# Optimization experiments

Measured on AMD Instinct MI355X. Metric: run time of the kernel, lower is better.

Reference implementation:

```python
import jax, jax.numpy as jnp
import numpy as np

SIZE = 7  # spatial size, matches init kwarg


def setup_inputs() -> dict:
    key = jax.random.key(0)
    k1, k2 = jax.random.split(key, 2)
    N, C, H, W = 256, 2048, SIZE, SIZE
    x = jax.random.normal(k1, (N, C, H, W), dtype=jnp.float32)
    # nn.Linear(2*C, 2): weight (2, 2C), bias (2,)
    Wlin = jax.random.normal(k2, (2, 2 * C), dtype=jnp.float32) * 0.02
    b = jnp.zeros((2,), dtype=jnp.float32)
    return {"x": x, "Wlin": Wlin, "b": b}


def reference(x, Wlin, b):
    N, C, H, W = x.shape
    HW = H * W
    size = SIZE
    # (N, HW, C) token view
    rx = x.reshape(N, C, HW).transpose(0, 2, 1)
    # index of max mean-activation token per sample
    idx = jnp.argmax(jnp.mean(rx, axis=-1), axis=-1)  # (N,)
    bidx = jnp.arange(N)
    max_feat = rx[bidx, idx]  # (N, C)
    # concat(max_feat, rx) @ Wlin.T + b, split to avoid materializing (N,HW,2C)
    W1, W2 = Wlin[:, :C], Wlin[:, C:]
    pred = jax.nn.relu(
        jnp.einsum('npc,oc->npo', rx, W2) + (max_feat @ W1.T)[:, None, :] + b
    )  # (N, HW, 2)
    # zero out prediction at the anchor token
    pred = pred.at[bidx, idx].set(0.0)
    # basic label grid (i, j)
    ii, jj = jnp.meshgrid(jnp.arange(H), jnp.arange(W), indexing='ij')
    label = jnp.stack([ii, jj], axis=-1).reshape(HW, 2).astype(x.dtype)  # (HW, 2)
    anchor = label[idx][:, None, :]  # (N, 1, 2)
    rel = (label[None, :, :] - anchor) / size  # (N, HW, 2)
    rel_dist = jnp.sqrt(jnp.sum(rel ** 2, axis=-1))  # (N, HW)
    rel_angle = (jnp.arctan2(rel[..., 1], rel[..., 0]) / jnp.pi + 1) / 2  # (N, HW)
    dist_loss = (pred[..., 0] - rel_dist) ** 2
    gap = pred[..., 1] - rel_angle
    gap = jnp.where(gap < 0, gap + 1, gap)
    gap = gap - jnp.mean(gap, axis=-1, keepdims=True)
    return (dist_loss + gap ** 2).reshape(N, H, W)
```

## Files before the change

### kernel.cpp

```cpp
#include <hip/hip_runtime.h>
#include <hip/hip_bf16.h>
#include <math.h>

#define N_BATCH 256
#define C_CH    2048
#define HW      49
#define SIZE7   7
#define S_SPLIT 8
#define C_PER   (C_CH / S_SPLIT)
#define BLOCK   256
#define WAVES   4

__global__ __launch_bounds__(BLOCK) void rpp_partial_kernel(
    const float* __restrict__ x, const float* __restrict__ Wlin,
    float* __restrict__ ws) {
  const int bid  = blockIdx.x;
  const int n    = bid >> 3;
  const int s    = bid & (S_SPLIT - 1);
  const int tid  = threadIdx.x;
  const int lane = tid & 63;
  const int wave = tid >> 6;

  __shared__ __align__(16) float w_s[4][C_PER];
  __shared__ float red[WAVES][5][64];

  const int cbase = s * C_PER;
  for (int i = tid; i < 4 * C_PER; i += BLOCK) {
    const int q = i >> 8;
    const int c = i & (C_PER - 1);
    const int off = (q & 1) * (2 * C_CH) + (q >> 1) * C_CH;
    w_s[q][c] = Wlin[off + cbase + c];
  }
  __syncthreads();

  const int lp = (lane < HW) ? lane : 0;
  const int wbase = wave * 64;
  const float* xp = x + (size_t)n * C_CH * HW + (size_t)(cbase + wbase) * HW + lp;

  float a0 = 0.f, a1 = 0.f, a2 = 0.f, a3 = 0.f, a4 = 0.f;
#pragma unroll 4
  for (int c = 0; c < 64; c += 4, xp += 4 * HW) {
    const float v0 = xp[0 * HW];
    const float v1 = xp[1 * HW];
    const float v2 = xp[2 * HW];
    const float v3 = xp[3 * HW];
    const float4 w0 = *(const float4*)&w_s[0][wbase + c];
    const float4 w1 = *(const float4*)&w_s[1][wbase + c];
    const float4 w2 = *(const float4*)&w_s[2][wbase + c];
    const float4 w3 = *(const float4*)&w_s[3][wbase + c];
    a0 += (v0 + v1) + (v2 + v3);
    a1 = fmaf(v0, w0.x, fmaf(v1, w0.y, fmaf(v2, w0.z, fmaf(v3, w0.w, a1))));
    a2 = fmaf(v0, w1.x, fmaf(v1, w1.y, fmaf(v2, w1.z, fmaf(v3, w1.w, a2))));
    a3 = fmaf(v0, w2.x, fmaf(v1, w2.y, fmaf(v2, w2.z, fmaf(v3, w2.w, a3))));
    a4 = fmaf(v0, w3.x, fmaf(v1, w3.y, fmaf(v2, w3.z, fmaf(v3, w3.w, a4))));
  }

  red[wave][0][lane] = a0;
  red[wave][1][lane] = a1;
  red[wave][2][lane] = a2;
  red[wave][3][lane] = a3;
  red[wave][4][lane] = a4;
  __syncthreads();

  for (int i = tid; i < 5 * 64; i += BLOCK) {
    const int q = i >> 6;
    const int l = i & 63;
    ws[(size_t)bid * 320 + i] =
        red[0][q][l] + red[1][q][l] + red[2][q][l] + red[3][q][l];
  }
}

__global__ __launch_bounds__(64) void rpp_final_kernel(
    const float* __restrict__ ws, const float* __restrict__ b,
    float* __restrict__ out) {
  const int n = blockIdx.x;
  const int lane = threadIdx.x;

  float s0 = 0.f, s1 = 0.f, s2 = 0.f, s3 = 0.f, s4 = 0.f;
  const float* base = ws + (size_t)n * S_SPLIT * 320;
#pragma unroll
  for (int s = 0; s < S_SPLIT; s++) {
    const float* bs = base + s * 320;
    s0 += bs[0 * 64 + lane];
    s1 += bs[1 * 64 + lane];
    s2 += bs[2 * 64 + lane];
    s3 += bs[3 * 64 + lane];
    s4 += bs[4 * 64 + lane];
  }

  float v = (lane < HW) ? s0 : -INFINITY;
  int vi = lane;
#pragma unroll
  for (int off = 32; off; off >>= 1) {
    const float ov = __shfl_down(v, off);
    const int oi = __shfl_down(vi, off);
    if (ov > v || (ov == v && oi < vi)) { v = ov; vi = oi; }
  }
  const int idx = __shfl(vi, 0);

  const float anc0 = __shfl(s1, idx);
  const float anc1 = __shfl(s2, idx);
  const float b0 = b[0], b1 = b[1];

  float pred0 = fmaxf(s3 + anc0 + b0, 0.f);
  float pred1 = fmaxf(s4 + anc1 + b1, 0.f);
  if (lane == idx) { pred0 = 0.f; pred1 = 0.f; }

  const int li = lane / SIZE7, lj = lane % SIZE7;
  const int ai = idx / SIZE7, aj = idx % SIZE7;
  const float ri = (float)(li - ai) * (1.0f / SIZE7);
  const float rj = (float)(lj - aj) * (1.0f / SIZE7);
  const float rdist = sqrtf(ri * ri + rj * rj);
  const float rangle = atan2f(rj, ri) * 0.15915494309189535f + 0.5f;

  float dl = pred0 - rdist;
  dl *= dl;
  float gap = pred1 - rangle;
  if (gap < 0.f) gap += 1.f;

  float g = (lane < HW) ? gap : 0.f;
#pragma unroll
  for (int off = 32; off; off >>= 1) g += __shfl_down(g, off);
  const float mean = __shfl(g, 0) * (1.0f / HW);
  gap -= mean;

  if (lane < HW) out[(size_t)n * HW + lane] = dl + gap * gap;
}

extern "C" void kernel_launch(void* const* d_in, const int* in_sizes, int n_in,
                              void* d_out, int out_size, void* d_ws, size_t ws_size,
                              hipStream_t stream) {
  const float* x    = (const float*)d_in[0];
  const float* Wlin = (const float*)d_in[1];
  const float* b    = (const float*)d_in[2];
  float* out = (float*)d_out;
  float* ws  = (float*)d_ws;

  hipLaunchKernelGGL(rpp_partial_kernel, dim3(N_BATCH * S_SPLIT), dim3(BLOCK), 0,
                     stream, x, Wlin, ws);
  hipLaunchKernelGGL(rpp_final_kernel, dim3(N_BATCH), dim3(64), 0,
                     stream, ws, b, out);
}
```

Measured before the change: 154.9 us.

## Fuse partial reduction and final loss into one 1024-thread block per sample

Replaces the split-channel partial kernel plus the final kernel with a single kernel in which one 1024-thread block handles a whole sample. The cross-block reduction moves into shared memory and the workspace round trip goes away. The inner loop is unrolled to eight channels per iteration. This removes a launch and the global intermediate, but leaves only one block per CU with fewer resident waves to hide memory latency.

```diff
diff --git a/kernel.cpp b/kernel.cpp
--- a/kernel.cpp
+++ b/kernel.cpp
@@ -1,58 +1,66 @@
 #include <hip/hip_runtime.h>
-#include <hip/hip_bf16.h>
 #include <math.h>
 
 #define N_BATCH 256
 #define C_CH    2048
 #define HW      49
 #define SIZE7   7
-#define S_SPLIT 8
-#define C_PER   (C_CH / S_SPLIT)
-#define BLOCK   256
-#define WAVES   4
+#define BLOCK   1024
+#define NWAVES  16
+#define C_PER_W (C_CH / NWAVES)
 
-__global__ __launch_bounds__(BLOCK) void rpp_partial_kernel(
+__global__ __launch_bounds__(BLOCK) void rpp_fused_kernel(
     const float* __restrict__ x, const float* __restrict__ Wlin,
-    float* __restrict__ ws) {
-  const int bid  = blockIdx.x;
-  const int n    = bid >> 3;
-  const int s    = bid & (S_SPLIT - 1);
+    const float* __restrict__ b, float* __restrict__ out) {
+  const int n    = blockIdx.x;
   const int tid  = threadIdx.x;
   const int lane = tid & 63;
   const int wave = tid >> 6;
 
-  __shared__ __align__(16) float w_s[4][C_PER];
-  __shared__ float red[WAVES][5][64];
+  __shared__ __align__(16) float w_s[4][C_CH];
+  __shared__ float red[NWAVES][5][64];
 
-  const int cbase = s * C_PER;
-  for (int i = tid; i < 4 * C_PER; i += BLOCK) {
-    const int q = i >> 8;
-    const int c = i & (C_PER - 1);
+  for (int i = tid; i < 4 * C_CH; i += BLOCK) {
+    const int q = i >> 11;
+    const int c = i & (C_CH - 1);
     const int off = (q & 1) * (2 * C_CH) + (q >> 1) * C_CH;
-    w_s[q][c] = Wlin[off + cbase + c];
+    w_s[q][c] = Wlin[off + c];
   }
   __syncthreads();
 
   const int lp = (lane < HW) ? lane : 0;
-  const int wbase = wave * 64;
-  const float* xp = x + (size_t)n * C_CH * HW + (size_t)(cbase + wbase) * HW + lp;
+  const int cb = wave * C_PER_W;
+  const float* xp = x + (size_t)n * C_CH * HW + (size_t)cb * HW + lp;
 
   float a0 = 0.f, a1 = 0.f, a2 = 0.f, a3 = 0.f, a4 = 0.f;
-#pragma unroll 4
-  for (int c = 0; c < 64; c += 4, xp += 4 * HW) {
+#pragma unroll 2
+  for (int c = 0; c < C_PER_W; c += 8) {
     const float v0 = xp[0 * HW];
     const float v1 = xp[1 * HW];
     const float v2 = xp[2 * HW];
     const float v3 = xp[3 * HW];
-    const float4 w0 = *(const float4*)&w_s[0][wbase + c];
-    const float4 w1 = *(const float4*)&w_s[1][wbase + c];
-    const float4 w2 = *(const float4*)&w_s[2][wbase + c];
-    const float4 w3 = *(const float4*)&w_s[3][wbase + c];
-    a0 += (v0 + v1) + (v2 + v3);
-    a1 = fmaf(v0, w0.x, fmaf(v1, w0.y, fmaf(v2, w0.z, fmaf(v3, w0.w, a1))));
-    a2 = fmaf(v0, w1.x, fmaf(v1, w1.y, fmaf(v2, w1.z, fmaf(v3, w1.w, a2))));
-    a3 = fmaf(v0, w2.x, fmaf(v1, w2.y, fmaf(v2, w2.z, fmaf(v3, w2.w, a3))));
-    a4 = fmaf(v0, w3.x, fmaf(v1, w3.y, fmaf(v2, w3.z, fmaf(v3, w3.w, a4))));
+    const float v4 = xp[4 * HW];
+    const float v5 = xp[5 * HW];
+    const float v6 = xp[6 * HW];
+    const float v7 = xp[7 * HW];
+    xp += 8 * HW;
+    const float4 wa0 = *(const float4*)&w_s[0][cb + c];
+    const float4 wa1 = *(const float4*)&w_s[0][cb + c + 4];
+    const float4 wb0 = *(const float4*)&w_s[1][cb + c];
+    const float4 wb1 = *(const float4*)&w_s[1][cb + c + 4];
+    const float4 wc0 = *(const float4*)&w_s[2][cb + c];
+    const float4 wc1 = *(const float4*)&w_s[2][cb + c + 4];
+    const float4 wd0 = *(const float4*)&w_s[3][cb + c];
+    const float4 wd1 = *(const float4*)&w_s[3][cb + c + 4];
+    a0 += ((v0 + v1) + (v2 + v3)) + ((v4 + v5) + (v6 + v7));
+    a1 = fmaf(v0, wa0.x, fmaf(v1, wa0.y, fmaf(v2, wa0.z, fmaf(v3, wa0.w, a1))));
+    a1 = fmaf(v4, wa1.x, fmaf(v5, wa1.y, fmaf(v6, wa1.z, fmaf(v7, wa1.w, a1))));
+    a2 = fmaf(v0, wb0.x, fmaf(v1, wb0.y, fmaf(v2, wb0.z, fmaf(v3, wb0.w, a2))));
+    a2 = fmaf(v4, wb1.x, fmaf(v5, wb1.y, fmaf(v6, wb1.z, fmaf(v7, wb1.w, a2))));
+    a3 = fmaf(v0, wc0.x, fmaf(v1, wc0.y, fmaf(v2, wc0.z, fmaf(v3, wc0.w, a3))));
+    a3 = fmaf(v4, wc1.x, fmaf(v5, wc1.y, fmaf(v6, wc1.z, fmaf(v7, wc1.w, a3))));
+    a4 = fmaf(v0, wd0.x, fmaf(v1, wd0.y, fmaf(v2, wd0.z, fmaf(v3, wd0.w, a4))));
+    a4 = fmaf(v4, wd1.x, fmaf(v5, wd1.y, fmaf(v6, wd1.z, fmaf(v7, wd1.w, a4))));
   }
 
   red[wave][0][lane] = a0;
@@ -62,69 +70,61 @@
   red[wave][4][lane] = a4;
   __syncthreads();
 
-  for (int i = tid; i < 5 * 64; i += BLOCK) {
-    const int q = i >> 6;
-    const int l = i & 63;
-    ws[(size_t)bid * 320 + i] =
-        red[0][q][l] + red[1][q][l] + red[2][q][l] + red[3][q][l];
+  if (tid < 5 * 64) {
+    const int q = tid >> 6;
+    const int l = tid & 63;
+    float s = 0.f;
+#pragma unroll
+    for (int w = 0; w < NWAVES; w++) s += red[w][q][l];
+    red[0][q][l] = s;
   }
-}
+  __syncthreads();
 
-__global__ __launch_bounds__(64) void rpp_final_kernel(
-    const float* __restrict__ ws, const float* __restrict__ b,
-    float* __restrict__ out) {
-  const int n = blockIdx.x;
-  const int lane = threadIdx.x;
+  if (wave == 0) {
+    const float s0 = red[0][0][lane];
+    const float s1 = red[0][1][lane];
+    const float s2 = red[0][2][lane];
+    const float s3 = red[0][3][lane];
+    const float s4 = red[0][4][lane];
 
-  float s0 = 0.f, s1 = 0.f, s2 = 0.f, s3 = 0.f, s4 = 0.f;
-  const float* base = ws + (size_t)n * S_SPLIT * 320;
+    float v = (lane < HW) ? s0 : -INFINITY;
+    int vi = lane;
 #pragma unroll
-  for (int s = 0; s < S_SPLIT; s++) {
-    const float* bs = base + s * 320;
-    s0 += bs[0 * 64 + lane];
-    s1 += bs[1 * 64 + lane];
-    s2 += bs[2 * 64 + lane];
-    s3 += bs[3 * 64 + lane];
-    s4 += bs[4 * 64 + lane];
+    for (int off = 32; off; off >>= 1) {
+      const float ov = __shfl_down(v, off);
+      const int oi = __shfl_down(vi, off);
+      if (ov > v || (ov == v && oi < vi)) { v = ov; vi = oi; }
+    }
+    const int idx = __shfl(vi, 0);
+
+    const float anc0 = __shfl(s1, idx);
+    const float anc1 = __shfl(s2, idx);
+    const float b0 = b[0], b1 = b[1];
+
+    float pred0 = fmaxf(s3 + anc0 + b0, 0.f);
+    float pred1 = fmaxf(s4 + anc1 + b1, 0.f);
+    if (lane == idx) { pred0 = 0.f; pred1 = 0.f; }
+
+    const int li = lane / SIZE7, lj = lane % SIZE7;
+    const int ai = idx / SIZE7, aj = idx % SIZE7;
+    const float ri = (float)(li - ai) * (1.0f / SIZE7);
+    const float rj = (float)(lj - aj) * (1.0f / SIZE7);
+    const float rdist = sqrtf(ri * ri + rj * rj);
+    const float rangle = atan2f(rj, ri) * 0.15915494309189535f + 0.5f;
+
+    float dl = pred0 - rdist;
+    dl *= dl;
+    float gap = pred1 - rangle;
+    if (gap < 0.f) gap += 1.f;
+
+    float g = (lane < HW) ? gap : 0.f;
+#pragma unroll
+    for (int off = 32; off; off >>= 1) g += __shfl_down(g, off);
+    const float mean = __shfl(g, 0) * (1.0f / HW);
+    gap -= mean;
+
+    if (lane < HW) out[(size_t)n * HW + lane] = dl + gap * gap;
   }
-
-  float v = (lane < HW) ? s0 : -INFINITY;
-  int vi = lane;
-#pragma unroll
-  for (int off = 32; off; off >>= 1) {
-    const float ov = __shfl_down(v, off);
-    const int oi = __shfl_down(vi, off);
-    if (ov > v || (ov == v && oi < vi)) { v = ov; vi = oi; }
-  }
-  const int idx = __shfl(vi, 0);
-
-  const float anc0 = __shfl(s1, idx);
-  const float anc1 = __shfl(s2, idx);
-  const float b0 = b[0], b1 = b[1];
-
-  float pred0 = fmaxf(s3 + anc0 + b0, 0.f);
-  float pred1 = fmaxf(s4 + anc1 + b1, 0.f);
-  if (lane == idx) { pred0 = 0.f; pred1 = 0.f; }
-
-  const int li = lane / SIZE7, lj = lane % SIZE7;
-  const int ai = idx / SIZE7, aj = idx % SIZE7;
-  const float ri = (float)(li - ai) * (1.0f / SIZE7);
-  const float rj = (float)(lj - aj) * (1.0f / SIZE7);
-  const float rdist = sqrtf(ri * ri + rj * rj);
-  const float rangle = atan2f(rj, ri) * 0.15915494309189535f + 0.5f;
-
-  float dl = pred0 - rdist;
-  dl *= dl;
-  float gap = pred1 - rangle;
-  if (gap < 0.f) gap += 1.f;
-
-  float g = (lane < HW) ? gap : 0.f;
-#pragma unroll
-  for (int off = 32; off; off >>= 1) g += __shfl_down(g, off);
-  const float mean = __shfl(g, 0) * (1.0f / HW);
-  gap -= mean;
-
-  if (lane < HW) out[(size_t)n * HW + lane] = dl + gap * gap;
 }
 
 extern "C" void kernel_launch(void* const* d_in, const int* in_sizes, int n_in,
@@ -134,10 +134,8 @@
   const float* Wlin = (const float*)d_in[1];
   const float* b    = (const float*)d_in[2];
   float* out = (float*)d_out;
-  float* ws  = (float*)d_ws;
+  (void)d_ws; (void)ws_size;
 
-  hipLaunchKernelGGL(rpp_partial_kernel, dim3(N_BATCH * S_SPLIT), dim3(BLOCK), 0,
-                     stream, x, Wlin, ws);
-  hipLaunchKernelGGL(rpp_final_kernel, dim3(N_BATCH), dim3(64), 0,
-                     stream, ws, b, out);
+  hipLaunchKernelGGL(rpp_fused_kernel, dim3(N_BATCH), dim3(BLOCK), 0,
+                     stream, x, Wlin, b, out);
 }
```

Result: no change. 153.7 us (-0.8%).
